# Kernel tuning notes

Measured on AMD Instinct MI355X. Metric: run time of the kernel, lower is better.

## Reference

```python
import jax, jax.numpy as jnp
import numpy as np

B = 2 ** 21          # batch of independent 3-qubit state vectors
NQ = 3               # qubits, state dim = 2**NQ = 8
INV_SQRT2 = np.float32(1.0 / np.sqrt(2.0))


def setup_inputs() -> dict:
    key = jax.random.key(0)
    k1, k2, k3, k4 = jax.random.split(key, 4)
    x_real = jax.random.normal(k1, (B, 8), jnp.float32)
    x_imag = jax.random.normal(k2, (B, 8), jnp.float32)
    theta = jax.random.normal(k3, (2,), jnp.float32)   # learned RX angles for qubits 0,1
    angle = jax.random.normal(k4, (1,), jnp.float32)   # dead arg (R built but never applied)
    return {"x_real": x_real, "x_imag": x_imag, "theta": theta, "angle": angle}


def _apply_1q(x, U, qubit):
    # x: (B,2,2,2) complex state, U: (2,2) gate, qubit in {0,1,2} -> axis qubit+1
    x = jnp.moveaxis(x, qubit + 1, -1)
    x = jnp.einsum('...j,ij->...i', x, U)
    return jnp.moveaxis(x, -1, qubit + 1)


def _circuit(x_real, x_imag, theta):
    x = (x_real + 1j * x_imag).astype(jnp.complex64).reshape(-1, 2, 2, 2)
    # Hadamard on qubits 0 and 1
    H = jnp.array([[1.0, 1.0], [1.0, -1.0]], jnp.complex64) * INV_SQRT2
    x = _apply_1q(x, H, 0)
    x = _apply_1q(x, H, 1)
    # RX(theta_q) = exp(-i theta sigma_x / 2) on qubits 0 and 1
    for q in (0, 1):
        c = jnp.cos(theta[q] * 0.5).astype(jnp.complex64)
        s = jnp.sin(theta[q] * 0.5).astype(jnp.complex64)
        RX = jnp.stack([jnp.stack([c, -1j * s]), jnp.stack([-1j * s, c])])
        x = _apply_1q(x, RX, q)
    # CNOT: control=qubit 0, target=qubit 2 (flip target axis when control=1)
    x = jnp.stack([x[:, 0], x[:, 1, :, ::-1]], axis=1)
    x = x.reshape(-1, 8)
    return jnp.stack([jnp.real(x), jnp.imag(x)], axis=-1)  # (B, 8, 2) float32


def reference(x_real, x_imag, theta, angle):
    # `angle` is dead code in the original forward (R created, never applied)
    return _circuit(x_real, x_imag, theta)
```

## Files before the change

### kernel.cpp

```cpp
#include <hip/hip_runtime.h>

__global__ __launch_bounds__(256) void circuit_kernel(
    const float* __restrict__ xr,
    const float* __restrict__ xi,
    const float* __restrict__ theta,
    float* __restrict__ out,
    int B)
{
    int t = blockIdx.x * blockDim.x + threadIdx.x;
    if (t >= B) return;

    const float k = 0.70710678118654752440f;
    float c0, s0, c1, s1;
    sincosf(theta[0] * 0.5f, &s0, &c0);
    sincosf(theta[1] * 0.5f, &s1, &c1);

    const float4* xr4 = reinterpret_cast<const float4*>(xr) + 2 * t;
    const float4* xi4 = reinterpret_cast<const float4*>(xi) + 2 * t;
    float4 ra = xr4[0], rb = xr4[1];
    float4 ia = xi4[0], ib = xi4[1];

    float r[8] = {ra.x, ra.y, ra.z, ra.w, rb.x, rb.y, rb.z, rb.w};
    float m[8] = {ia.x, ia.y, ia.z, ia.w, ib.x, ib.y, ib.z, ib.w};

#pragma unroll
    for (int i = 0; i < 4; ++i) {
        float ar = r[i], am = m[i], br = r[i + 4], bm = m[i + 4];
        r[i]     = k * (ar + br);  m[i]     = k * (am + bm);
        r[i + 4] = k * (ar - br);  m[i + 4] = k * (am - bm);
    }
#pragma unroll
    for (int j = 0; j < 4; ++j) {
        int i = (j & 1) | ((j >> 1) << 2);
        float ar = r[i], am = m[i], br = r[i + 2], bm = m[i + 2];
        r[i]     = k * (ar + br);  m[i]     = k * (am + bm);
        r[i + 2] = k * (ar - br);  m[i + 2] = k * (am - bm);
    }
#pragma unroll
    for (int i = 0; i < 4; ++i) {
        float ar = r[i], am = m[i], br = r[i + 4], bm = m[i + 4];
        r[i]     = c0 * ar + s0 * bm;
        m[i]     = c0 * am - s0 * br;
        r[i + 4] = c0 * br + s0 * am;
        m[i + 4] = c0 * bm - s0 * ar;
    }
#pragma unroll
    for (int j = 0; j < 4; ++j) {
        int i = (j & 1) | ((j >> 1) << 2);
        float ar = r[i], am = m[i], br = r[i + 2], bm = m[i + 2];
        r[i]     = c1 * ar + s1 * bm;
        m[i]     = c1 * am - s1 * br;
        r[i + 2] = c1 * br + s1 * am;
        m[i + 2] = c1 * bm - s1 * ar;
    }
    {
        float tr = r[4]; r[4] = r[5]; r[5] = tr;
        float tm = m[4]; m[4] = m[5]; m[5] = tm;
        tr = r[6]; r[6] = r[7]; r[7] = tr;
        tm = m[6]; m[6] = m[7]; m[7] = tm;
    }

    float4* o4 = reinterpret_cast<float4*>(out) + 4 * t;
    o4[0] = make_float4(r[0], m[0], r[1], m[1]);
    o4[1] = make_float4(r[2], m[2], r[3], m[3]);
    o4[2] = make_float4(r[4], m[4], r[5], m[5]);
    o4[3] = make_float4(r[6], m[6], r[7], m[7]);
}

extern "C" void kernel_launch(void* const* d_in, const int* in_sizes, int n_in,
                              void* d_out, int out_size, void* d_ws, size_t ws_size,
                              hipStream_t stream) {
    const float* xr    = (const float*)d_in[0];
    const float* xi    = (const float*)d_in[1];
    const float* theta = (const float*)d_in[2];
    float* out = (float*)d_out;

    int B = in_sizes[0] / 8;
    int block = 256;
    int grid = (B + block - 1) / block;
    circuit_kernel<<<grid, block, 0, stream>>>(xr, xi, theta, out, B);
}
```

Baseline: 243.4 us.

## Split each state across two lanes and fold H·RX into fused complex gates

Each 8-element state is now handled by two adjacent threads, each loading one float4 per input and exchanging partial results with a lane shuffle. The Hadamard and RX gates on each qubit are combined algebraically into single complex multiplies, which cuts the arithmetic. Intrinsic __sincosf replaces sincosf. The intent is more in-flight memory requests per thread group and less ALU work in a bandwidth-bound kernel, at the cost of doubling the thread count and adding shuffles.

```diff
diff --git a/kernel.cpp b/kernel.cpp
--- a/kernel.cpp
+++ b/kernel.cpp
@@ -1,82 +1,73 @@
 #include <hip/hip_runtime.h>
 
 __global__ __launch_bounds__(256) void circuit_kernel(
-    const float* __restrict__ xr,
-    const float* __restrict__ xi,
+    const float4* __restrict__ xr4,
+    const float4* __restrict__ xi4,
     const float* __restrict__ theta,
-    float* __restrict__ out,
-    int B)
+    float4* __restrict__ o4,
+    int N)
 {
-    int t = blockIdx.x * blockDim.x + threadIdx.x;
-    if (t >= B) return;
+    int u = blockIdx.x * blockDim.x + threadIdx.x;
+    if (u >= N) return;
+    const int h = u & 1;
+    const float k = 0.70710678118654752440f;
 
-    const float k = 0.70710678118654752440f;
     float c0, s0, c1, s1;
-    sincosf(theta[0] * 0.5f, &s0, &c0);
-    sincosf(theta[1] * 0.5f, &s1, &c1);
+    __sincosf(theta[0] * 0.5f, &s0, &c0);
+    __sincosf(theta[1] * 0.5f, &s1, &c1);
 
-    const float4* xr4 = reinterpret_cast<const float4*>(xr) + 2 * t;
-    const float4* xi4 = reinterpret_cast<const float4*>(xi) + 2 * t;
-    float4 ra = xr4[0], rb = xr4[1];
-    float4 ia = xi4[0], ib = xi4[1];
+    const float mr = k * c0;
+    const float mi = h ? (k * s0) : (-k * s0);
 
-    float r[8] = {ra.x, ra.y, ra.z, ra.w, rb.x, rb.y, rb.z, rb.w};
-    float m[8] = {ia.x, ia.y, ia.z, ia.w, ib.x, ib.y, ib.z, ib.w};
+    float4 fr = xr4[u];
+    float4 fi = xi4[u];
+    float ar[4] = {fr.x, fr.y, fr.z, fr.w};
+    float ai[4] = {fi.x, fi.y, fi.z, fi.w};
 
+    float lr[4], li[4], pr[4], pi[4];
 #pragma unroll
-    for (int i = 0; i < 4; ++i) {
-        float ar = r[i], am = m[i], br = r[i + 4], bm = m[i + 4];
-        r[i]     = k * (ar + br);  m[i]     = k * (am + bm);
-        r[i + 4] = k * (ar - br);  m[i + 4] = k * (am - bm);
+    for (int j = 0; j < 4; ++j) {
+        lr[j] = mr * ar[j] - mi * ai[j];
+        li[j] = mr * ai[j] + mi * ar[j];
     }
 #pragma unroll
     for (int j = 0; j < 4; ++j) {
-        int i = (j & 1) | ((j >> 1) << 2);
-        float ar = r[i], am = m[i], br = r[i + 2], bm = m[i + 2];
-        r[i]     = k * (ar + br);  m[i]     = k * (am + bm);
-        r[i + 2] = k * (ar - br);  m[i + 2] = k * (am - bm);
-    }
-#pragma unroll
-    for (int i = 0; i < 4; ++i) {
-        float ar = r[i], am = m[i], br = r[i + 4], bm = m[i + 4];
-        r[i]     = c0 * ar + s0 * bm;
-        m[i]     = c0 * am - s0 * br;
-        r[i + 4] = c0 * br + s0 * am;
-        m[i + 4] = c0 * bm - s0 * ar;
+        pr[j] = __shfl_xor(lr[j], 1, 64);
+        pi[j] = __shfl_xor(li[j], 1, 64);
     }
 #pragma unroll
     for (int j = 0; j < 4; ++j) {
-        int i = (j & 1) | ((j >> 1) << 2);
-        float ar = r[i], am = m[i], br = r[i + 2], bm = m[i + 2];
-        r[i]     = c1 * ar + s1 * bm;
-        m[i]     = c1 * am - s1 * br;
-        r[i + 2] = c1 * br + s1 * am;
-        m[i + 2] = c1 * bm - s1 * ar;
-    }
-    {
-        float tr = r[4]; r[4] = r[5]; r[5] = tr;
-        float tm = m[4]; m[4] = m[5]; m[5] = tm;
-        tr = r[6]; r[6] = r[7]; r[7] = tr;
-        tm = m[6]; m[6] = m[7]; m[7] = tm;
+        ar[j] = h ? (pr[j] - lr[j]) : (lr[j] + pr[j]);
+        ai[j] = h ? (pi[j] - li[j]) : (li[j] + pi[j]);
     }
 
-    float4* o4 = reinterpret_cast<float4*>(out) + 4 * t;
-    o4[0] = make_float4(r[0], m[0], r[1], m[1]);
-    o4[1] = make_float4(r[2], m[2], r[3], m[3]);
-    o4[2] = make_float4(r[4], m[4], r[5], m[5]);
-    o4[3] = make_float4(r[6], m[6], r[7], m[7]);
+    const float p1r = k * c1, p1i = -k * s1;
+    const float q1r = k * c1, q1i = k * s1;
+#pragma unroll
+    for (int j = 0; j < 2; ++j) {
+        float xr_ = p1r * ar[j]     - p1i * ai[j];
+        float xi_ = p1r * ai[j]     + p1i * ar[j];
+        float yr_ = q1r * ar[j + 2] - q1i * ai[j + 2];
+        float yi_ = q1r * ai[j + 2] + q1i * ar[j + 2];
+        ar[j]     = xr_ + yr_;  ai[j]     = xi_ + yi_;
+        ar[j + 2] = xr_ - yr_;  ai[j + 2] = xi_ - yi_;
+    }
+
+    int a = h ? 1 : 0, b = h ? 0 : 1, c = h ? 3 : 2, d = h ? 2 : 3;
+    o4[2 * u]     = make_float4(ar[a], ai[a], ar[b], ai[b]);
+    o4[2 * u + 1] = make_float4(ar[c], ai[c], ar[d], ai[d]);
 }
 
 extern "C" void kernel_launch(void* const* d_in, const int* in_sizes, int n_in,
                               void* d_out, int out_size, void* d_ws, size_t ws_size,
                               hipStream_t stream) {
-    const float* xr    = (const float*)d_in[0];
-    const float* xi    = (const float*)d_in[1];
+    const float4* xr4  = (const float4*)d_in[0];
+    const float4* xi4  = (const float4*)d_in[1];
     const float* theta = (const float*)d_in[2];
-    float* out = (float*)d_out;
+    float4* o4 = (float4*)d_out;
 
-    int B = in_sizes[0] / 8;
+    int N = in_sizes[0] / 4;
     int block = 256;
-    int grid = (B + block - 1) / block;
-    circuit_kernel<<<grid, block, 0, stream>>>(xr, xi, theta, out, B);
+    int grid = (N + block - 1) / block;
+    circuit_kernel<<<grid, block, 0, stream>>>(xr4, xi4, theta, o4, N);
 }
```

Result: no change. 240.7 us (-1.1%).
